# Kernel tuning notes

Hardware: AMD Instinct MI355X
Metric: run time of the kernel (lower is better)

The kernel has to match this reference:

```python
import jax, jax.numpy as jnp
import numpy as np

K = 7  # kernel_size from init


def setup_inputs() -> dict:
    key = jax.random.key(0)
    ks = jax.random.split(key, 4)
    B, C, H, W = 8, 64, 384, 384
    x = jax.random.normal(ks[0], (B, C, H, W), dtype=jnp.float32)
    w1 = jax.random.normal(ks[1], (16, C), dtype=jnp.float32) * (1.0 / np.sqrt(C))
    b1 = jnp.zeros((16,), dtype=jnp.float32)
    w2 = jax.random.normal(ks[2], (3, 16), dtype=jnp.float32) * 0.25
    b2 = jnp.zeros((3,), dtype=jnp.float32)
    return {"x": x, "w1": w1, "b1": b1, "w2": w2, "b2": b2}


def reference(x, w1, b1, w2, b2):
    B, C, H, W = x.shape
    # param predictor: global avg pool -> 1x1 conv (dense) -> SiLU -> 1x1 conv (dense)
    pooled = x.mean(axis=(2, 3))                       # [B, C]
    h = jax.nn.silu(pooled @ w1.T + b1)                # [B, 16]
    p = h @ w2.T + b2                                  # [B, 3]
    sigma = jax.nn.softplus(p[:, 0])                   # [B]
    dx = jnp.tanh(p[:, 1]) * 2.0
    dy = jnp.tanh(p[:, 2]) * 2.0
    # per-sample Gaussian kernels, vectorized over batch
    coords = jnp.arange(K, dtype=x.dtype)
    gy, gx = jnp.meshgrid(coords, coords, indexing="ij")  # [K, K]
    cx = (K - 1) / 2.0 + dx                            # [B]
    cy = (K - 1) / 2.0 + dy
    g = jnp.exp(-((gx[None] - cx[:, None, None]) ** 2 + (gy[None] - cy[:, None, None]) ** 2)
                / (2.0 * sigma[:, None, None] ** 2))   # [B, K, K]
    g = g / g.sum(axis=(1, 2), keepdims=True)
    # depthwise conv with per-sample kernel via groups = B*C
    kernels = jnp.broadcast_to(g[:, None], (B, C, K, K)).reshape(B * C, 1, K, K)
    out = jax.lax.conv_general_dilated(
        x.reshape(1, B * C, H, W), kernels,
        window_strides=(1, 1), padding=[(K // 2, K // 2)] * 2,
        feature_group_count=B * C,
        dimension_numbers=("NCHW", "OIHW", "NCHW"))
    return out.reshape(B, C, H, W)
```

## Files before the change

kernel.cpp:

```cpp
#include <hip/hip_runtime.h>
#include <math.h>

#define IMG_W 384
#define IMG_H 384
#define IMG_HW (IMG_W * IMG_H)
#define N_IMG 512
#define N_CH 64
#define N_B 8

__global__ __launch_bounds__(256) void pool_kernel(const float* __restrict__ x,
                                                   float* __restrict__ pooled) {
    const int bc = blockIdx.x;
    const float4* xp = (const float4*)(x + (size_t)bc * IMG_HW);
    const int t = threadIdx.x;
    float s = 0.f;
    #pragma unroll 4
    for (int k = 0; k < 144; ++k) {
        float4 v = xp[t + k * 256];
        s += (v.x + v.y) + (v.z + v.w);
    }
    #pragma unroll
    for (int off = 32; off > 0; off >>= 1) s += __shfl_down(s, off, 64);
    __shared__ float red[4];
    if ((t & 63) == 0) red[t >> 6] = s;
    __syncthreads();
    if (t == 0) {
        float tot = (red[0] + red[1]) + (red[2] + red[3]);
        pooled[bc] = tot * (1.0f / (float)IMG_HW);
    }
}

__global__ void params_kernel(const float* __restrict__ pooled,
                              const float* __restrict__ w1, const float* __restrict__ b1,
                              const float* __restrict__ w2, const float* __restrict__ b2,
                              float* __restrict__ guv) {
    const int b = threadIdx.x;
    if (b >= N_B) return;
    const float* P = pooled + b * N_CH;
    float h[16];
    #pragma unroll
    for (int j = 0; j < 16; ++j) {
        float acc = b1[j];
        for (int c = 0; c < N_CH; ++c) acc += P[c] * w1[j * N_CH + c];
        h[j] = acc / (1.f + expf(-acc));
    }
    float p[3];
    #pragma unroll
    for (int k = 0; k < 3; ++k) {
        float acc = b2[k];
        #pragma unroll
        for (int j = 0; j < 16; ++j) acc += h[j] * w2[k * 16 + j];
        p[k] = acc;
    }
    float sigma = (p[0] > 20.f) ? p[0] : log1pf(expf(p[0]));
    float dx = tanhf(p[1]) * 2.f;
    float dy = tanhf(p[2]) * 2.f;
    float cx = 3.f + dx, cy = 3.f + dy;
    float inv2s2 = 1.f / (2.f * sigma * sigma);
    float u[7], v[7], su = 0.f, sv = 0.f;
    #pragma unroll
    for (int i = 0; i < 7; ++i) { float d = (float)i - cx; u[i] = expf(-d * d * inv2s2); su += u[i]; }
    #pragma unroll
    for (int j = 0; j < 7; ++j) { float d = (float)j - cy; v[j] = expf(-d * d * inv2s2); sv += v[j]; }
    float rsu = 1.f / su, rsv = 1.f / sv;
    #pragma unroll
    for (int i = 0; i < 7; ++i) guv[b * 14 + i] = u[i] * rsu;
    #pragma unroll
    for (int j = 0; j < 7; ++j) guv[b * 14 + 7 + j] = v[j] * rsv;
}

__global__ __launch_bounds__(384) void conv_kernel(const float* __restrict__ x,
                                                   const float* __restrict__ guv,
                                                   float* __restrict__ out) {
    __shared__ float buf[2][8][392];
    const int tid = threadIdx.x;
    const int bc = blockIdx.x;
    const int b = bc >> 6;
    const float* img = x + (size_t)bc * IMG_HW;
    float* oimg = out + (size_t)bc * IMG_HW;

    float u[7], v[7];
    #pragma unroll
    for (int i = 0; i < 7; ++i) { u[i] = guv[b * 14 + i]; v[i] = guv[b * 14 + 7 + i]; }

    if (tid < 128) {
        int r = tid >> 3;
        int p = tid & 7;
        int col = (p < 4) ? p : (384 + p);
        buf[r >> 3][r & 7][col] = 0.f;
    }

    for (int q = tid; q < 576; q += 384) {
        int brow = q / 96;
        int c4 = (q % 96) * 4;
        int row = -3 + brow;
        float4 val = make_float4(0.f, 0.f, 0.f, 0.f);
        if (row >= 0) val = *(const float4*)(img + row * IMG_W + c4);
        *(float4*)&buf[1][brow][4 + c4] = val;
    }
    #pragma unroll
    for (int k = 0; k < 2; ++k) {
        int q = tid + k * 384;
        int brow = q / 96;
        int c4 = (q % 96) * 4;
        float4 val = *(const float4*)(img + (3 + brow) * IMG_W + c4);
        *(float4*)&buf[0][brow][4 + c4] = val;
    }
    __syncthreads();

    const int xc = tid + 1;
    float h[6];
    #pragma unroll
    for (int k = 0; k < 6; ++k) {
        float a = 0.f;
        #pragma unroll
        for (int i = 0; i < 7; ++i) a += u[i] * buf[1][k][xc + i];
        h[k] = a;
    }

    for (int c = 0; c < 48; ++c) {
        __syncthreads();
        float4 nv[2];
        int brow_[2], c4_[2];
        const bool have_next = (c + 1 < 48);
        if (have_next) {
            int r0 = 8 * (c + 1) + 3;
            #pragma unroll
            for (int k = 0; k < 2; ++k) {
                int q = tid + k * 384;
                brow_[k] = q / 96;
                c4_[k] = (q % 96) * 4;
                int row = r0 + brow_[k];
                nv[k] = make_float4(0.f, 0.f, 0.f, 0.f);
                if (row < IMG_H) nv[k] = *(const float4*)(img + row * IMG_W + c4_[k]);
            }
        }
        const float (*bufc)[392] = buf[c & 1];
        const int ybase = 8 * c;
        #pragma unroll
        for (int r = 0; r < 8; ++r) {
            float hn = 0.f;
            #pragma unroll
            for (int i = 0; i < 7; ++i) hn += u[i] * bufc[r][xc + i];
            float o = v[0] * h[0] + v[1] * h[1] + v[2] * h[2] + v[3] * h[3]
                    + v[4] * h[4] + v[5] * h[5] + v[6] * hn;
            oimg[(ybase + r) * IMG_W + tid] = o;
            #pragma unroll
            for (int k = 0; k < 5; ++k) h[k] = h[k + 1];
            h[5] = hn;
        }
        if (have_next) {
            float (*bufn)[392] = buf[(c + 1) & 1];
            #pragma unroll
            for (int k = 0; k < 2; ++k) {
                *(float4*)&bufn[brow_[k]][4 + c4_[k]] = nv[k];
            }
        }
    }
}

extern "C" void kernel_launch(void* const* d_in, const int* in_sizes, int n_in,
                              void* d_out, int out_size, void* d_ws, size_t ws_size,
                              hipStream_t stream) {
    const float* x  = (const float*)d_in[0];
    const float* w1 = (const float*)d_in[1];
    const float* b1 = (const float*)d_in[2];
    const float* w2 = (const float*)d_in[3];
    const float* b2 = (const float*)d_in[4];
    float* outp = (float*)d_out;

    float* pooled = (float*)d_ws;
    float* guv    = pooled + 512;

    pool_kernel<<<N_IMG, 256, 0, stream>>>(x, pooled);
    params_kernel<<<1, 64, 0, stream>>>(pooled, w1, b1, w2, b2, guv);
    conv_kernel<<<N_IMG, 384, 0, stream>>>(x, guv, outp);
}
```

Measured before the change: 598.6 us.

## Split conv into row bands per image and reverse image order for cache reuse

The depthwise conv kernel now launches four blocks per image, each handling a 96-row band with a 3-row halo, instead of one block sweeping all 384 rows. This raises the block count from 512 to 2048 to fill the GPU's compute units better and shorten the serial per-block chain. Images are also processed in reverse order, so the last images read by the pooling kernel, which may still sit in cache, are convolved first. The cost is extra halo loads per band and one more horizontal-prologue pass per block.

After: 602.2 us. Within noise of the previous version (+0.6%).

```diff
diff --git a/kernel.cpp b/kernel.cpp
--- a/kernel.cpp
+++ b/kernel.cpp
@@ -7,6 +7,9 @@
 #define N_IMG 512
 #define N_CH 64
 #define N_B 8
+#define BAND_ROWS 96
+#define N_BANDS 4
+#define CHUNKS_PER_BAND 12
 
 __global__ __launch_bounds__(256) void pool_kernel(const float* __restrict__ x,
                                                    float* __restrict__ pooled) {
@@ -74,10 +77,12 @@
                                                    float* __restrict__ out) {
     __shared__ float buf[2][8][392];
     const int tid = threadIdx.x;
-    const int bc = blockIdx.x;
-    const int b = bc >> 6;
-    const float* img = x + (size_t)bc * IMG_HW;
-    float* oimg = out + (size_t)bc * IMG_HW;
+    const int img = (N_IMG - 1) - (blockIdx.x >> 2);
+    const int band = blockIdx.x & 3;
+    const int y0 = band * BAND_ROWS;
+    const int b = img >> 6;
+    const float* imgp = x + (size_t)img * IMG_HW;
+    float* oimg = out + (size_t)img * IMG_HW;
 
     float u[7], v[7];
     #pragma unroll
@@ -93,9 +98,9 @@
     for (int q = tid; q < 576; q += 384) {
         int brow = q / 96;
         int c4 = (q % 96) * 4;
-        int row = -3 + brow;
+        int row = y0 - 3 + brow;
         float4 val = make_float4(0.f, 0.f, 0.f, 0.f);
-        if (row >= 0) val = *(const float4*)(img + row * IMG_W + c4);
+        if (row >= 0) val = *(const float4*)(imgp + row * IMG_W + c4);
         *(float4*)&buf[1][brow][4 + c4] = val;
     }
     #pragma unroll
@@ -103,7 +108,9 @@
         int q = tid + k * 384;
         int brow = q / 96;
         int c4 = (q % 96) * 4;
-        float4 val = *(const float4*)(img + (3 + brow) * IMG_W + c4);
+        int row = y0 + 3 + brow;
+        float4 val = make_float4(0.f, 0.f, 0.f, 0.f);
+        if (row < IMG_H) val = *(const float4*)(imgp + row * IMG_W + c4);
         *(float4*)&buf[0][brow][4 + c4] = val;
     }
     __syncthreads();
@@ -118,13 +125,13 @@
         h[k] = a;
     }
 
-    for (int c = 0; c < 48; ++c) {
+    for (int c = 0; c < CHUNKS_PER_BAND; ++c) {
         __syncthreads();
         float4 nv[2];
         int brow_[2], c4_[2];
-        const bool have_next = (c + 1 < 48);
+        const bool have_next = (c + 1 < CHUNKS_PER_BAND);
         if (have_next) {
-            int r0 = 8 * (c + 1) + 3;
+            int r0 = y0 + 8 * (c + 1) + 3;
             #pragma unroll
             for (int k = 0; k < 2; ++k) {
                 int q = tid + k * 384;
@@ -132,11 +139,11 @@
                 c4_[k] = (q % 96) * 4;
                 int row = r0 + brow_[k];
                 nv[k] = make_float4(0.f, 0.f, 0.f, 0.f);
-                if (row < IMG_H) nv[k] = *(const float4*)(img + row * IMG_W + c4_[k]);
+                if (row < IMG_H) nv[k] = *(const float4*)(imgp + row * IMG_W + c4_[k]);
             }
         }
         const float (*bufc)[392] = buf[c & 1];
-        const int ybase = 8 * c;
+        const int ybase = y0 + 8 * c;
         #pragma unroll
         for (int r = 0; r < 8; ++r) {
             float hn = 0.f;
@@ -174,5 +181,5 @@
 
     pool_kernel<<<N_IMG, 256, 0, stream>>>(x, pooled);
     params_kernel<<<1, 64, 0, stream>>>(pooled, w1, b1, w2, b2, guv);
-    conv_kernel<<<N_IMG, 384, 0, stream>>>(x, guv, outp);
+    conv_kernel<<<N_IMG * N_BANDS, 384, 0, stream>>>(x, guv, outp);
 }
```
